# Kernel tuning notes

Measured on AMD Instinct MI355X. Metric: run time of the kernel, lower is better.

The kernel has to match this reference:

```python
import jax, jax.numpy as jnp
import numpy as np

N_NODES = 50000
N_EDGES = 1600000


def _seg_softmax(e, seg, n):
    # numerically-stable softmax over edges grouped by destination node
    m = jax.ops.segment_max(e, seg, num_segments=n)
    ex = jnp.exp(e - m[seg])
    s = jax.ops.segment_sum(ex, seg, num_segments=n)
    return ex / s[seg]


def setup_inputs() -> dict:
    key = jax.random.key(0)
    ks = jax.random.split(key, 16)
    IN, OUT, ED = 64, 32, 8
    inp = {
        'x': jax.random.normal(ks[0], (N_NODES, IN), jnp.float32),
        'ex': jax.random.normal(ks[1], (N_EDGES, ED), jnp.float32),
        'src': jax.random.randint(ks[2], (N_EDGES,), 0, N_NODES),
        'dst': jax.random.randint(ks[3], (N_EDGES,), 0, N_NODES),
        'W_fc': jax.random.normal(ks[4], (OUT, IN), jnp.float32) * 0.1,
        'b_fc': jax.random.normal(ks[5], (OUT,), jnp.float32) * 0.1,
        'W_att': jax.random.normal(ks[6], (1, 2 * OUT + ED), jnp.float32) * 0.1,
        'b_att': jax.random.normal(ks[7], (1,), jnp.float32) * 0.1,
        'W_edge': jax.random.normal(ks[8], (OUT, ED), jnp.float32) * 0.1,
        'b_edge': jax.random.normal(ks[9], (OUT,), jnp.float32) * 0.1,
        'W_eatt': jax.random.normal(ks[10], (ED, ED), jnp.float32) * 0.1,
        'b_eatt': jax.random.normal(ks[11], (ED,), jnp.float32) * 0.1,
        'W_q': jax.random.normal(ks[12], (OUT, OUT), jnp.float32) * 0.1,
        'b_q': jax.random.normal(ks[13], (OUT,), jnp.float32) * 0.1,
        'W_s': jax.random.normal(ks[14], (OUT, OUT), jnp.float32) * 0.1,
        'b_s': jax.random.normal(ks[15], (OUT,), jnp.float32) * 0.1,
    }
    return inp


def reference(x, ex, src, dst, W_fc, b_fc, W_att, b_att, W_edge, b_edge,
              W_eatt, b_eatt, W_q, b_q, W_s, b_s):
    n = x.shape[0]
    # node transform (fc; batch norm disabled in config)
    z = x @ W_fc.T + b_fc                      # [N, OUT]
    z_src = z[src]                             # [E, OUT]
    z_dst = z[dst]                             # [E, OUT]
    # edge transform for attention score
    ex_t = ex @ W_eatt.T + b_eatt              # [E, ED]
    # edge-dependent attention logit + leaky_relu(0.2)
    z2 = jnp.concatenate([z_src, z_dst, ex_t], axis=1)  # [E, 2*OUT+ED]
    a = z2 @ W_att.T + b_att                   # [E, 1]
    e = jnp.where(a >= 0, a, 0.2 * a)
    # edge feature aggregation transform
    ez = ex @ W_edge.T + b_edge                # [E, OUT]
    # similar_node branch: pointwise conv1d == linear; per-edge dot product
    q = z_src @ W_q.T + b_q                    # query(src)
    s = z_dst @ W_s.T + b_s                    # support(dst)
    es = jnp.sum(q * s, axis=1, keepdims=True)  # [E, 1]
    # edge-softmax over incoming edges of each destination node
    alpha = _seg_softmax(e, dst, n)            # [E, 1]
    similar = _seg_softmax(es, dst, n)         # [E, 1]
    h_att = jax.ops.segment_sum(alpha * z_src, dst, num_segments=n)    # [N, OUT]
    h2 = jax.ops.segment_sum(similar * z_src, dst, num_segments=n)     # [N, OUT]
    h = h_att * h2
    # attention-weighted edge feature aggregation
    h = h + jax.ops.segment_sum(alpha * ez, dst, num_segments=n)
    return h, alpha
```

## Files before the change

### kernel.cpp

```cpp
#include <hip/hip_runtime.h>
#include <hip/hip_fp16.h>

#define OUTF 32
#define INF 64
#define EDF 8
#define CAP 64
#define BSH 7
#define NBKMAX 512
#define EPB 4096

__global__ __launch_bounds__(256) void prep_kernel(
    const float* __restrict__ x,
    const float* __restrict__ W_fc, const float* __restrict__ b_fc,
    const float* __restrict__ W_q,  const float* __restrict__ b_q,
    const float* __restrict__ W_s,  const float* __restrict__ b_s,
    const float* __restrict__ W_att,
    __half* __restrict__ qz, float* __restrict__ s,
    float* __restrict__ att_s, float* __restrict__ att_d,
    int* __restrict__ cursor, int* __restrict__ bhist, int n_nodes)
{
    int i = blockIdx.x * 256 + threadIdx.x;
    if (i < NBKMAX) bhist[i] = 0;
    if (i >= n_nodes) return;
    cursor[i] = i * CAP;
    int n = i;

    float xl[INF];
    for (int k = 0; k < INF; k++) xl[k] = x[(size_t)n * INF + k];

    float zl[OUTF];
    float a1 = 0.f, a2 = 0.f;
    for (int o = 0; o < OUTF; o++) {
        float acc = b_fc[o];
        for (int k = 0; k < INF; k++) acc += xl[k] * W_fc[o * INF + k];
        zl[o] = acc;
        qz[(size_t)n * 64 + 32 + o] = __float2half(acc);
        a1 += acc * W_att[o];
        a2 += acc * W_att[OUTF + o];
    }
    att_s[n] = a1;
    att_d[n] = a2;

    for (int o = 0; o < OUTF; o++) {
        float aq = b_q[o], as = b_s[o];
        for (int k = 0; k < OUTF; k++) {
            aq += zl[k] * W_q[o * OUTF + k];
            as += zl[k] * W_s[o * OUTF + k];
        }
        qz[(size_t)n * 64 + o] = __float2half(aq);
        s[(size_t)n * OUTF + o] = as;
    }
}

__global__ __launch_bounds__(256) void bhist_kernel(
    const int* __restrict__ didx, int* __restrict__ bhist, int eBase, int eEnd)
{
    __shared__ int cnt[NBKMAX];
    for (int i = threadIdx.x; i < NBKMAX; i += 256) cnt[i] = 0;
    __syncthreads();
    int e0 = eBase + blockIdx.x * EPB;
    #pragma unroll 16
    for (int k = 0; k < 16; k++) {
        int e = e0 + k * 256 + threadIdx.x;
        if (e < eEnd) atomicAdd(&cnt[didx[e] >> BSH], 1);
    }
    __syncthreads();
    for (int i = threadIdx.x; i < NBKMAX; i += 256)
        if (cnt[i]) atomicAdd(&bhist[i], cnt[i]);
}

__global__ __launch_bounds__(512) void bscan_kernel(
    int* __restrict__ bhist, int* __restrict__ bbase,
    int* __restrict__ bcursor, int nbk)
{
    __shared__ int sh[512];
    int t = threadIdx.x;
    int v = (t < nbk) ? bhist[t] : 0;
    sh[t] = v;
    __syncthreads();
    for (int st = 1; st < 512; st <<= 1) {
        int tv = (t >= st) ? sh[t - st] : 0;
        __syncthreads();
        sh[t] += tv;
        __syncthreads();
    }
    if (t < nbk) {
        int excl = sh[t] - v;
        bbase[t] = excl;
        bcursor[t] = excl;
        bhist[t] = 0;
        if (t == nbk - 1) bbase[nbk] = sh[t];
    }
}

__global__ __launch_bounds__(256) void bin_kernel(
    const int* __restrict__ sidx, const int* __restrict__ didx,
    int* __restrict__ bcursor, int2* __restrict__ stage, int eBase, int eEnd)
{
    __shared__ int cnt[NBKMAX];
    __shared__ int gbase[NBKMAX];
    for (int i = threadIdx.x; i < NBKMAX; i += 256) cnt[i] = 0;
    __syncthreads();
    int e0 = eBase + blockIdx.x * EPB;
    int srcv[16], dstv[16], rankv[16];
    #pragma unroll 16
    for (int k = 0; k < 16; k++) {
        int e = e0 + k * 256 + threadIdx.x;
        if (e < eEnd) {
            srcv[k] = sidx[e]; dstv[k] = didx[e];
            rankv[k] = atomicAdd(&cnt[dstv[k] >> BSH], 1);
        } else srcv[k] = -1;
    }
    __syncthreads();
    for (int b = threadIdx.x; b < NBKMAX; b += 256)
        if (cnt[b]) gbase[b] = atomicAdd(&bcursor[b], cnt[b]);
    __syncthreads();
    #pragma unroll 16
    for (int k = 0; k < 16; k++) {
        if (srcv[k] >= 0) {
            int e = e0 + k * 256 + threadIdx.x;
            int b = dstv[k] >> BSH;
            stage[gbase[b] + rankv[k]] =
                make_int2(srcv[k], e | ((dstv[k] & 127) << 21));
        }
    }
}

__global__ __launch_bounds__(256) void place_kernel(
    const int* __restrict__ bbase, const int2* __restrict__ stage,
    int2* __restrict__ csr, int* __restrict__ cursor, int N)
{
    __shared__ int c[1 << BSH];
    int b = blockIdx.x;
    int nodeBase = b << BSH;
    int nNodes = min(1 << BSH, N - nodeBase);
    for (int i = threadIdx.x; i < nNodes; i += 256) c[i] = cursor[nodeBase + i];
    __syncthreads();
    int beg = bbase[b], end = bbase[b + 1];
    for (int j = beg + threadIdx.x; j < end; j += 256) {
        int2 r = stage[j];
        int dl  = (r.y >> 21) & 127;
        int eid = r.y & 0x1FFFFF;
        int pos = atomicAdd(&c[dl], 1);
        if (pos < (nodeBase + dl) * CAP + CAP)
            csr[pos] = make_int2(r.x, eid);
    }
    __syncthreads();
    for (int i = threadIdx.x; i < nNodes; i += 256) {
        int lim = (nodeBase + i) * CAP + CAP;
        cursor[nodeBase + i] = min(c[i], lim);
    }
}

__device__ __forceinline__ float4 loadHalf4(const __half* p) {
    uint2 raw = *(const uint2*)p;
    __half2 h01 = *reinterpret_cast<__half2*>(&raw.x);
    __half2 h23 = *reinterpret_cast<__half2*>(&raw.y);
    float2 f01 = __half22float2(h01);
    float2 f23 = __half22float2(h23);
    return make_float4(f01.x, f01.y, f23.x, f23.y);
}

__global__ __launch_bounds__(256) void agg_kernel(
    const int* __restrict__ cursor, const int2* __restrict__ csr,
    const float* __restrict__ att_d,
    const __half* __restrict__ qz, const float* __restrict__ s,
    const float* __restrict__ ex,
    const float* __restrict__ W_att, const float* __restrict__ b_att,
    const float* __restrict__ W_eatt, const float* __restrict__ b_eatt,
    const float* __restrict__ W_edge, const float* __restrict__ b_edge,
    float* __restrict__ h_out, float* __restrict__ invS_out, int N)
{
    __shared__ float sv3[EDF];
    __shared__ float ccs;
    __shared__ float sWedge[OUTF * EDF];
    __shared__ float sbedge[OUTF];
    int tid = threadIdx.x;
    if (tid < EDF) {
        float a = 0.f;
        for (int j = 0; j < EDF; j++) a += W_att[2 * OUTF + j] * W_eatt[j * EDF + tid];
        sv3[tid] = a;
    }
    if (tid == 0) {
        float a = b_att[0];
        for (int j = 0; j < EDF; j++) a += W_att[2 * OUTF + j] * b_eatt[j];
        ccs = a;
    }
    if (tid < OUTF * EDF) sWedge[tid] = W_edge[tid];
    if (tid < OUTF) sbedge[tid] = b_edge[tid];
    __syncthreads();

    int wave = blockIdx.x * 4 + (tid >> 6);
    if (wave >= N) return;
    int lane = tid & 63;
    int g = lane >> 3;
    int l = lane & 7;
    int n = wave;
    int beg = n * CAP, end = cursor[n];

    float4 s4  = *(const float4*)(s + (size_t)n * OUTF + l * 4);
    float4 wa4 = *(const float4*)(W_att + l * 4);
    float4 v34 = (l < 2) ? *(const float4*)(sv3 + l * 4)
                         : make_float4(0.f, 0.f, 0.f, 0.f);
    float attc = att_d[n] + ccs;

    float S = 0.f, Spe = 0.f;
    float4 U1 = make_float4(0.f, 0.f, 0.f, 0.f);
    float4 U2 = U1, Uax = U1;

    for (int p0 = beg; p0 < end; p0 += 16) {
        int posA = p0 + g;
        bool vA = posA < end;
        int2 ceA = csr[vA ? posA : beg];
        int posB = p0 + 8 + g;
        bool vB = posB < end;
        int2 ceB = csr[vB ? posB : beg];

        const __half* rowA = qz + (size_t)ceA.x * 64;
        const __half* rowB = qz + (size_t)ceB.x * 64;
        float4 qA = loadHalf4(rowA + l * 4);
        float4 zA = loadHalf4(rowA + 32 + l * 4);
        float4 qB = loadHalf4(rowB + l * 4);
        float4 zB = loadHalf4(rowB + 32 + l * 4);
        float4 eA = (l < 2) ? *(const float4*)(ex + (size_t)ceA.y * EDF + l * 4)
                            : make_float4(0.f, 0.f, 0.f, 0.f);
        float4 eB = (l < 2) ? *(const float4*)(ex + (size_t)ceB.y * EDF + l * 4)
                            : make_float4(0.f, 0.f, 0.f, 0.f);

        float rA = qA.x * s4.x + qA.y * s4.y + qA.z * s4.z + qA.w * s4.w;
        float mA = zA.x * wa4.x + zA.y * wa4.y + zA.z * wa4.z + zA.w * wa4.w
                 + eA.x * v34.x + eA.y * v34.y + eA.z * v34.z + eA.w * v34.w;
        float rB = qB.x * s4.x + qB.y * s4.y + qB.z * s4.z + qB.w * s4.w;
        float mB = zB.x * wa4.x + zB.y * wa4.y + zB.z * wa4.z + zB.w * wa4.w
                 + eB.x * v34.x + eB.y * v34.y + eB.z * v34.z + eB.w * v34.w;
        #pragma unroll
        for (int m = 4; m >= 1; m >>= 1) {
            rA += __shfl_xor(rA, m);
            mA += __shfl_xor(mA, m);
            rB += __shfl_xor(rB, m);
            mB += __shfl_xor(mB, m);
        }
        float aA = mA + attc;
        float aB = mB + attc;
        float pA  = vA ? __expf(aA >= 0.f ? aA : 0.2f * aA) : 0.f;
        float peA = vA ? __expf(rA) : 0.f;
        float pB  = vB ? __expf(aB >= 0.f ? aB : 0.2f * aB) : 0.f;
        float peB = vB ? __expf(rB) : 0.f;

        S += pA + pB; Spe += peA + peB;
        U1.x += pA * zA.x + pB * zB.x;  U1.y += pA * zA.y + pB * zB.y;
        U1.z += pA * zA.z + pB * zB.z;  U1.w += pA * zA.w + pB * zB.w;
        U2.x += peA * zA.x + peB * zB.x; U2.y += peA * zA.y + peB * zB.y;
        U2.z += peA * zA.z + peB * zB.z; U2.w += peA * zA.w + peB * zB.w;
        Uax.x += pA * eA.x + pB * eB.x; Uax.y += pA * eA.y + pB * eB.y;
        Uax.z += pA * eA.z + pB * eB.z; Uax.w += pA * eA.w + pB * eB.w;
    }

    #pragma unroll
    for (int m = 8; m <= 32; m <<= 1) {
        S   += __shfl_xor(S, m);
        Spe += __shfl_xor(Spe, m);
        U1.x += __shfl_xor(U1.x, m); U1.y += __shfl_xor(U1.y, m);
        U1.z += __shfl_xor(U1.z, m); U1.w += __shfl_xor(U1.w, m);
        U2.x += __shfl_xor(U2.x, m); U2.y += __shfl_xor(U2.y, m);
        U2.z += __shfl_xor(U2.z, m); U2.w += __shfl_xor(U2.w, m);
        Uax.x += __shfl_xor(Uax.x, m); Uax.y += __shfl_xor(Uax.y, m);
        Uax.z += __shfl_xor(Uax.z, m); Uax.w += __shfl_xor(Uax.w, m);
    }

    float invS = 0.f;
    float4 h4 = make_float4(0.f, 0.f, 0.f, 0.f);
    if (end > beg) {
        invS = 1.f / S;
        float invSpe = 1.f / Spe;
        float ax[EDF];
        ax[0] = __shfl(Uax.x, 0); ax[1] = __shfl(Uax.y, 0);
        ax[2] = __shfl(Uax.z, 0); ax[3] = __shfl(Uax.w, 0);
        ax[4] = __shfl(Uax.x, 1); ax[5] = __shfl(Uax.y, 1);
        ax[6] = __shfl(Uax.z, 1); ax[7] = __shfl(Uax.w, 1);
        #pragma unroll
        for (int j = 0; j < 4; j++) {
            int c = l * 4 + j;
            float hagg = sbedge[c];
            #pragma unroll
            for (int k = 0; k < EDF; k++)
                hagg += sWedge[c * EDF + k] * (ax[k] * invS);
            float hatt = ((j == 0) ? U1.x : (j == 1) ? U1.y : (j == 2) ? U1.z : U1.w) * invS;
            float h2   = ((j == 0) ? U2.x : (j == 1) ? U2.y : (j == 2) ? U2.z : U2.w) * invSpe;
            ((float*)&h4)[j] = hatt * h2 + hagg;
        }
    }
    if (lane < 8) {
        *(float4*)(h_out + (size_t)n * OUTF + l * 4) = h4;
        if (lane == 0) invS_out[n] = invS;
    }
}

__global__ __launch_bounds__(256) void alpha_kernel(
    const int* __restrict__ sidx, const int* __restrict__ didx,
    const float* __restrict__ ex,
    const float* __restrict__ att_s, const float* __restrict__ att_d,
    const float* __restrict__ invS,
    const float* __restrict__ W_att, const float* __restrict__ b_att,
    const float* __restrict__ W_eatt, const float* __restrict__ b_eatt,
    float* __restrict__ alpha_out, int E)
{
    __shared__ float v3[EDF];
    __shared__ float ccs;
    int tid = threadIdx.x;
    if (tid < EDF) {
        float a = 0.f;
        for (int j = 0; j < EDF; j++) a += W_att[2 * OUTF + j] * W_eatt[j * EDF + tid];
        v3[tid] = a;
    }
    if (tid == 0) {
        float a = b_att[0];
        for (int j = 0; j < EDF; j++) a += W_att[2 * OUTF + j] * b_eatt[j];
        ccs = a;
    }
    __syncthreads();

    int e = blockIdx.x * 256 + tid;
    if (e >= E) return;
    int si = sidx[e], di = didx[e];
    const float4* exr = (const float4*)(ex + (size_t)e * EDF);
    float4 e0 = exr[0], e1 = exr[1];
    float a = att_s[si] + att_d[di] + ccs
            + e0.x * v3[0] + e0.y * v3[1] + e0.z * v3[2] + e0.w * v3[3]
            + e1.x * v3[4] + e1.y * v3[5] + e1.z * v3[6] + e1.w * v3[7];
    float el = (a >= 0.f) ? a : 0.2f * a;
    alpha_out[e] = __expf(el) * invS[di];
}

extern "C" void kernel_launch(void* const* d_in, const int* in_sizes, int n_in,
                              void* d_out, int out_size, void* d_ws, size_t ws_size,
                              hipStream_t stream) {
    const float* x      = (const float*)d_in[0];
    const float* ex     = (const float*)d_in[1];
    const int*   sidx   = (const int*)d_in[2];
    const int*   didx   = (const int*)d_in[3];
    const float* W_fc   = (const float*)d_in[4];
    const float* b_fc   = (const float*)d_in[5];
    const float* W_att  = (const float*)d_in[6];
    const float* b_att  = (const float*)d_in[7];
    const float* W_edge = (const float*)d_in[8];
    const float* b_edge = (const float*)d_in[9];
    const float* W_eatt = (const float*)d_in[10];
    const float* b_eatt = (const float*)d_in[11];
    const float* W_q    = (const float*)d_in[12];
    const float* b_q    = (const float*)d_in[13];
    const float* W_s    = (const float*)d_in[14];
    const float* b_s    = (const float*)d_in[15];

    int N = in_sizes[0] / INF;
    int E = in_sizes[2];
    int N32 = N * OUTF;
    int nbk = (N + (1 << BSH) - 1) >> BSH;

    float* h_out     = (float*)d_out;
    float* alpha_out = h_out + N32;

    float*  base    = (float*)d_ws;
    int*    cursor  = (int*)base;
    float*  att_s   = base + N;
    float*  att_d   = att_s + N;
    float*  invS    = att_d + N;
    __half* qz      = (__half*)(invS + N);
    float*  wsn     = (float*)(qz + (size_t)N * 64);
    size_t fixedBytes = (size_t)(4 * N) * 4 + (size_t)N * 64 * 2
                      + (size_t)N32 * 4 + (size_t)N * CAP * 8 + 8192;
    int halfE = (E + 1) / 2;
    int stageElems = (ws_size >= fixedBytes + (size_t)E * 8) ? E : halfE;
    int phases = (stageElems == E) ? 1 : 2;

    int2*  stage   = (int2*)(wsn + N32);
    int2*  csr     = stage + stageElems;
    int*   bhist   = (int*)(csr + (size_t)N * CAP);
    int*   bbase   = bhist + NBKMAX;
    int*   bcursor = bbase + NBKMAX + 1;

    prep_kernel<<<(N + 255) / 256, 256, 0, stream>>>(
        x, W_fc, b_fc, W_q, b_q, W_s, b_s, W_att,
        qz, wsn, att_s, att_d, cursor, bhist, N);

    for (int ph = 0; ph < phases; ph++) {
        int eB = ph * stageElems;
        int eE = (eB + stageElems < E) ? eB + stageElems : E;
        int nbC = (eE - eB + EPB - 1) / EPB;
        bhist_kernel<<<nbC, 256, 0, stream>>>(didx, bhist, eB, eE);
        bscan_kernel<<<1, 512, 0, stream>>>(bhist, bbase, bcursor, nbk);
        bin_kernel<<<nbC, 256, 0, stream>>>(sidx, didx, bcursor, stage, eB, eE);
        place_kernel<<<nbk, 256, 0, stream>>>(bbase, stage, csr, cursor, N);
    }

    int nbAgg = (N + 3) / 4;
    agg_kernel<<<nbAgg, 256, 0, stream>>>(
        cursor, csr, att_d,
        qz, wsn, ex,
        W_att, b_att, W_eatt, b_eatt, W_edge, b_edge,
        h_out, invS, N);

    int nbE = (E + 255) / 256;
    alpha_kernel<<<nbE, 256, 0, stream>>>(
        sidx, didx, ex, att_s, att_d, invS,
        W_att, b_att, W_eatt, b_eatt, alpha_out, E);
}
```

Measured before the change: 217.2 us.

## Fold query projection into per-destination vector to halve gathered row size

```diff
diff --git a/kernel.cpp b/kernel.cpp
--- a/kernel.cpp
+++ b/kernel.cpp
@@ -15,7 +15,8 @@
     const float* __restrict__ W_q,  const float* __restrict__ b_q,
     const float* __restrict__ W_s,  const float* __restrict__ b_s,
     const float* __restrict__ W_att,
-    __half* __restrict__ qz, float* __restrict__ s,
+    __half* __restrict__ z16, float* __restrict__ t,
+    float* __restrict__ c_es,
     float* __restrict__ att_s, float* __restrict__ att_d,
     int* __restrict__ cursor, int* __restrict__ bhist, int n_nodes)
 {
@@ -34,21 +35,26 @@
         float acc = b_fc[o];
         for (int k = 0; k < INF; k++) acc += xl[k] * W_fc[o * INF + k];
         zl[o] = acc;
-        qz[(size_t)n * 64 + 32 + o] = __float2half(acc);
+        z16[(size_t)n * OUTF + o] = __float2half(acc);
         a1 += acc * W_att[o];
         a2 += acc * W_att[OUTF + o];
     }
     att_s[n] = a1;
     att_d[n] = a2;
 
+    float sl[OUTF];
+    float ces = 0.f;
     for (int o = 0; o < OUTF; o++) {
-        float aq = b_q[o], as = b_s[o];
-        for (int k = 0; k < OUTF; k++) {
-            aq += zl[k] * W_q[o * OUTF + k];
-            as += zl[k] * W_s[o * OUTF + k];
-        }
-        qz[(size_t)n * 64 + o] = __float2half(aq);
-        s[(size_t)n * OUTF + o] = as;
+        float as = b_s[o];
+        for (int k = 0; k < OUTF; k++) as += zl[k] * W_s[o * OUTF + k];
+        sl[o] = as;
+        ces += b_q[o] * as;
+    }
+    c_es[n] = ces;
+    for (int k = 0; k < OUTF; k++) {
+        float tv = 0.f;
+        for (int o = 0; o < OUTF; o++) tv += W_q[o * OUTF + k] * sl[o];
+        t[(size_t)n * OUTF + k] = tv;
     }
 }
 
@@ -163,8 +169,8 @@
 
 __global__ __launch_bounds__(256) void agg_kernel(
     const int* __restrict__ cursor, const int2* __restrict__ csr,
-    const float* __restrict__ att_d,
-    const __half* __restrict__ qz, const float* __restrict__ s,
+    const float* __restrict__ att_d, const float* __restrict__ c_es,
+    const __half* __restrict__ z16, const float* __restrict__ t,
     const float* __restrict__ ex,
     const float* __restrict__ W_att, const float* __restrict__ b_att,
     const float* __restrict__ W_eatt, const float* __restrict__ b_eatt,
@@ -198,11 +204,12 @@
     int n = wave;
     int beg = n * CAP, end = cursor[n];
 
-    float4 s4  = *(const float4*)(s + (size_t)n * OUTF + l * 4);
+    float4 t4  = *(const float4*)(t + (size_t)n * OUTF + l * 4);
     float4 wa4 = *(const float4*)(W_att + l * 4);
     float4 v34 = (l < 2) ? *(const float4*)(sv3 + l * 4)
                          : make_float4(0.f, 0.f, 0.f, 0.f);
     float attc = att_d[n] + ccs;
+    float cesn = c_es[n];
 
     float S = 0.f, Spe = 0.f;
     float4 U1 = make_float4(0.f, 0.f, 0.f, 0.f);
@@ -216,21 +223,17 @@
         bool vB = posB < end;
         int2 ceB = csr[vB ? posB : beg];
 
-        const __half* rowA = qz + (size_t)ceA.x * 64;
-        const __half* rowB = qz + (size_t)ceB.x * 64;
-        float4 qA = loadHalf4(rowA + l * 4);
-        float4 zA = loadHalf4(rowA + 32 + l * 4);
-        float4 qB = loadHalf4(rowB + l * 4);
-        float4 zB = loadHalf4(rowB + 32 + l * 4);
+        float4 zA = loadHalf4(z16 + (size_t)ceA.x * OUTF + l * 4);
+        float4 zB = loadHalf4(z16 + (size_t)ceB.x * OUTF + l * 4);
         float4 eA = (l < 2) ? *(const float4*)(ex + (size_t)ceA.y * EDF + l * 4)
                             : make_float4(0.f, 0.f, 0.f, 0.f);
         float4 eB = (l < 2) ? *(const float4*)(ex + (size_t)ceB.y * EDF + l * 4)
                             : make_float4(0.f, 0.f, 0.f, 0.f);
 
-        float rA = qA.x * s4.x + qA.y * s4.y + qA.z * s4.z + qA.w * s4.w;
+        float rA = zA.x * t4.x + zA.y * t4.y + zA.z * t4.z + zA.w * t4.w;
         float mA = zA.x * wa4.x + zA.y * wa4.y + zA.z * wa4.z + zA.w * wa4.w
                  + eA.x * v34.x + eA.y * v34.y + eA.z * v34.z + eA.w * v34.w;
-        float rB = qB.x * s4.x + qB.y * s4.y + qB.z * s4.z + qB.w * s4.w;
+        float rB = zB.x * t4.x + zB.y * t4.y + zB.z * t4.z + zB.w * t4.w;
         float mB = zB.x * wa4.x + zB.y * wa4.y + zB.z * wa4.z + zB.w * wa4.w
                  + eB.x * v34.x + eB.y * v34.y + eB.z * v34.z + eB.w * v34.w;
         #pragma unroll
@@ -243,9 +246,9 @@
         float aA = mA + attc;
         float aB = mB + attc;
         float pA  = vA ? __expf(aA >= 0.f ? aA : 0.2f * aA) : 0.f;
-        float peA = vA ? __expf(rA) : 0.f;
+        float peA = vA ? __expf(rA + cesn) : 0.f;
         float pB  = vB ? __expf(aB >= 0.f ? aB : 0.2f * aB) : 0.f;
-        float peB = vB ? __expf(rB) : 0.f;
+        float peB = vB ? __expf(rB + cesn) : 0.f;
 
         S += pA + pB; Spe += peA + peB;
         U1.x += pA * zA.x + pB * zB.x;  U1.y += pA * zA.y + pB * zB.y;
@@ -365,15 +368,16 @@
     float*  att_s   = base + N;
     float*  att_d   = att_s + N;
     float*  invS    = att_d + N;
-    __half* qz      = (__half*)(invS + N);
-    float*  wsn     = (float*)(qz + (size_t)N * 64);
-    size_t fixedBytes = (size_t)(4 * N) * 4 + (size_t)N * 64 * 2
-                      + (size_t)N32 * 4 + (size_t)N * CAP * 8 + 8192;
+    float*  c_es    = invS + N;
+    __half* z16     = (__half*)(c_es + N);
+    float*  t       = (float*)(z16 + (size_t)N * OUTF);
+
+    size_t fixedBytes = (size_t)N * (20 + 64 + 128 + CAP * 8) + 8192;
     int halfE = (E + 1) / 2;
     int stageElems = (ws_size >= fixedBytes + (size_t)E * 8) ? E : halfE;
     int phases = (stageElems == E) ? 1 : 2;
 
-    int2*  stage   = (int2*)(wsn + N32);
+    int2*  stage   = (int2*)(t + N32);
     int2*  csr     = stage + stageElems;
     int*   bhist   = (int*)(csr + (size_t)N * CAP);
     int*   bbase   = bhist + NBKMAX;
@@ -381,7 +385,7 @@
 
     prep_kernel<<<(N + 255) / 256, 256, 0, stream>>>(
         x, W_fc, b_fc, W_q, b_q, W_s, b_s, W_att,
-        qz, wsn, att_s, att_d, cursor, bhist, N);
+        z16, t, c_es, att_s, att_d, cursor, bhist, N);
 
     for (int ph = 0; ph < phases; ph++) {
         int eB = ph * stageElems;
@@ -395,8 +399,8 @@
 
     int nbAgg = (N + 3) / 4;
     agg_kernel<<<nbAgg, 256, 0, stream>>>(
-        cursor, csr, att_d,
-        qz, wsn, ex,
+        cursor, csr, att_d, c_es,
+        z16, t, ex,
         W_att, b_att, W_eatt, b_eatt, W_edge, b_edge,
         h_out, invS, N);
 
```

Result: faster. 188.1 us (-13.4%).
